# Kernel optimization log

Hardware: AMD Instinct MI355X
Metric: run time of the kernel (lower is better)

## Reference

```python
import jax, jax.numpy as jnp
import numpy as np

CK = 16          # ck_size
REP50 = 50       # extra_feature.repeat(1, 50)
BN_EPS = 1e-5
SLOPE = 0.01     # LeakyReLU default slope

def leaky(x):
    return jnp.where(x >= 0, x, SLOPE * x)

def bn(x):
    # BatchNorm1d(affine=False, track_running_stats=False): per-call batch stats
    m = jnp.mean(x, axis=0, keepdims=True)
    v = jnp.var(x, axis=0, keepdims=True)
    return (x - m) * jax.lax.rsqrt(v + BN_EPS)

def rev_within(x, lengths):
    # reverse each sequence within its valid length, keep padding in place
    B, T, _ = x.shape
    t = jnp.arange(T)[None, :]
    idx = jnp.where(t < lengths[:, None], lengths[:, None] - 1 - t, t)
    return jnp.take_along_axis(x, idx[:, :, None], axis=1)

def lstm(x, lengths, Wih, Whh, bih, bhh):
    # masked unidirectional LSTM; padded steps output zeros (pad_packed behavior)
    B, T, D = x.shape
    H = Whh.shape[1]
    xg = jnp.einsum('btd,gd->btg', x, Wih) + bih + bhh             # [B,T,4H]
    mask = (jnp.arange(T)[None, :] < lengths[:, None])[..., None]  # [B,T,1]
    def step(carry, inp):
        h, c = carry
        g, m = inp
        g = g + h @ Whh.T
        i, f, gg, o = jnp.split(g, 4, axis=-1)  # torch gate order i,f,g,o
        c_new = jax.nn.sigmoid(f) * c + jax.nn.sigmoid(i) * jnp.tanh(gg)
        h_new = jax.nn.sigmoid(o) * jnp.tanh(c_new)
        h = jnp.where(m, h_new, h)
        c = jnp.where(m, c_new, c)
        return (h, c), h_new * m
    init = (jnp.zeros((B, H), x.dtype), jnp.zeros((B, H), x.dtype))
    _, outs = jax.lax.scan(step, init, (xg.transpose(1, 0, 2), mask.transpose(1, 0, 2)))
    return outs.transpose(1, 0, 2)  # [B,T,H]

def att_var(inputs, lengths, s1_w, s1_b, s2_w):
    # NOTE: faithful to source softmax_by_length, which (due to the original
    # code) normalizes the *raw* masked logits linearly; exp() is discarded.
    B, T, D = inputs.shape
    utt = leaky(bn(inputs.reshape(-1, D) @ s1_w.T + s1_b))
    alpha = (utt @ s2_w.T).reshape(B, T)
    m = (jnp.arange(T)[None, :] < lengths[:, None]).astype(alpha.dtype)
    am = alpha * m
    alpha_ = am / (jnp.sum(am, axis=1, keepdims=True) + 1e-9)
    return jnp.einsum('bt,btd->bd', alpha_, inputs)

def item_att(x, y):
    # x: [D], y: [N, D] -> [N, 3D+1]
    xb = jnp.broadcast_to(x, y.shape)
    dist = jnp.linalg.norm(xb - y, axis=-1, keepdims=True)
    return jnp.concatenate([xb, y, dist, xb * y], axis=-1)


def setup_inputs() -> dict:
    key = jax.random.key(0)
    ks = jax.random.split(key, 30)
    D, T, B = 1024, 128, 256
    Ne, Nc, P = 64, 128, 50
    Hh = D // 2
    f32 = jnp.float32
    def rn(k, shape, s=0.05):
        return jax.random.normal(k, shape, f32) * s
    inp = {}
    inp['word_encode'] = jax.random.normal(ks[0], (B, T, D), f32)
    inp['pos_encode'] = jax.random.normal(ks[1], (Ne, Nc // CK, P), f32)
    inp['dis_encode'] = jax.random.normal(ks[2], (Ne, Nc, P), f32)
    sl = jax.random.randint(ks[3], (B,), T // 2, T + 1)
    inp['sen_lengths'] = sl.at[0].set(T)
    inp['label3'] = jax.random.randint(ks[4], (Ne, 3), -1, Nc)
    inp['emo_idx'] = jnp.arange(Ne)
    inp['cau_idx'] = jnp.arange(Ne, Ne + Nc)
    # BiLSTM params (torch layout: [4H, in])
    inp['Wih_f'] = rn(ks[5], (4 * Hh, D)); inp['Whh_f'] = rn(ks[6], (4 * Hh, Hh))
    inp['bih_f'] = rn(ks[7], (4 * Hh,));  inp['bhh_f'] = rn(ks[8], (4 * Hh,))
    inp['Wih_b'] = rn(ks[9], (4 * Hh, D)); inp['Whh_b'] = rn(ks[10], (4 * Hh, Hh))
    inp['bih_b'] = rn(ks[11], (4 * Hh,)); inp['bhh_b'] = rn(ks[12], (4 * Hh,))
    # attention / projection params
    inp['s1_w'] = rn(ks[13], (D, D)); inp['s1_b'] = rn(ks[14], (D,))
    inp['s2_w'] = rn(ks[15], (1, D))
    inp['W2_w'] = rn(ks[16], (D, 3 * D + 1 + P)); inp['W2_b'] = rn(ks[17], (D,))
    inp['Wo_w'] = rn(ks[18], (2, D)); inp['Wo_b'] = rn(ks[19], (2,))
    inp['W3_w'] = rn(ks[20], (D, 3 * D + 51 + P)); inp['W3_b'] = rn(ks[21], (D,))
    inp['cls_w'] = rn(ks[22], (2, D)); inp['cls_b'] = rn(ks[23], (2,))
    return inp


def reference(word_encode, pos_encode, dis_encode,
              Wih_f, Whh_f, bih_f, bhh_f, Wih_b, Whh_b, bih_b, bhh_b,
              s1_w, s1_b, s2_w, W2_w, W2_b, Wo_w, Wo_b, W3_w, W3_b, cls_w, cls_b,
              sen_lengths, label3, emo_idx, cau_idx):
    lengths = sen_lengths
    out_f = lstm(word_encode, lengths, Wih_f, Whh_f, bih_f, bhh_f)
    out_b = rev_within(lstm(rev_within(word_encode, lengths), lengths,
                            Wih_b, Whh_b, bih_b, bhh_b), lengths)
    Hseq = jnp.concatenate([out_f, out_b], axis=-1)          # [B,T,D]
    U = att_var(Hseq, lengths, s1_w, s1_b, s2_w)             # [B,D]
    text_emo = U[emo_idx]                                    # [Ne,D]
    text_cau = U[cau_idx]                                    # [Nc,D]
    Nc, D = text_cau.shape
    Ne = text_emo.shape[0]
    cau_chunks = text_cau.reshape(Nc // CK, CK, D)           # [Nck,CK,D]

    # ground-truth cause labels per emotion (label3 -> binary over cau utts)
    valid = (label3 >= 0)
    safe = jnp.where(valid, label3, 0)
    L = jnp.zeros((Ne, Nc), U.dtype).at[jnp.arange(Ne)[:, None], safe].max(valid.astype(U.dtype))

    def per_emo(emo, pos_j, dis_j):
        # phase-2: chunk-level attention + classification
        sc = jax.nn.softmax(jnp.einsum('d,ncd->nc', emo, cau_chunks), axis=1)
        chunkEmb = jnp.einsum('nc,ncd->nd', sc, cau_chunks)          # [Nck,D]
        delta = jnp.concatenate([item_att(emo, chunkEmb), pos_j], -1)
        hidden = leaky(bn(delta @ W2_w.T + W2_b))
        out2 = jax.nn.log_softmax(hidden @ Wo_w.T + Wo_b, axis=-1)   # [Nck,2]
        # phase-3: utterance-level with chunk prediction as extra feature
        extra = jnp.repeat(jnp.argmax(out2, axis=-1).astype(emo.dtype), CK)[:, None]
        delta_ = jnp.concatenate([item_att(emo, text_cau), dis_j,
                                  jnp.tile(extra, (1, REP50))], -1)
        h = leaky(bn(delta_ @ W3_w.T + W3_b))
        p = jax.nn.log_softmax(h @ cls_w.T + cls_b, axis=-1)         # [Nc,2]
        return out2, p

    phase2, p3 = jax.vmap(per_emo)(text_emo, pos_encode, dis_encode)
    return phase2, p3, L
```

## Files before the change

kernel.cpp:

```cpp
#include <hip/hip_runtime.h>
#include <math.h>

#define DD    1024
#define TT    128
#define BB    256
#define NE    64
#define NCC   128
#define PPP   50
#define NCK   8
#define HH    512
#define G4    2048
#define NROWS 32768
#define K3PAD 3200
#define CHUNK 8

#define F_HSEQ  0ull
#define F_XG    33554432ull
#define F_WIH   41943040ull
#define F_WHH   46137344ull
#define F_S1    48234496ull
#define F_W2    49283072ull
#define F_W3    52559872ull
#define F_BIASC 56885248ull
#define F_HST   56889344ull
#define F_CST   57413632ull
#define F_CS    57675776ull
#define F_CSQ   57676800ull
#define F_BNM   57677824ull
#define F_BNI   57678848ull
#define F_ALPHA 57679872ull
#define F_U     57712640ull
#define F_H2    57974784ull
#define F_BN2M  58499072ull
#define F_BN2I  58564608ull
#define F_EXTRA 58630144ull
#define F_BN3M  58631168ull
#define F_BN3I  58696704ull

#define F_D2    F_HSEQ
#define F_CHE   (F_HSEQ + 26214400ull)
#define F_D3    F_HSEQ
#define F_H3    F_XG

typedef short s8v __attribute__((ext_vector_type(8)));
typedef float f4v __attribute__((ext_vector_type(4)));

__device__ __forceinline__ float leakyf(float x) { return x >= 0.f ? x : 0.01f * x; }
__device__ __forceinline__ float sigmf(float x)  { return 1.f / (1.f + __expf(-x)); }
__device__ __forceinline__ float tanhfast(float x) {
  float e = __expf(2.f * x);
  return 1.f - 2.f / (e + 1.f);
}

__device__ __forceinline__ float blk_sum(float v, float* s4) {
  for (int o = 32; o > 0; o >>= 1) v += __shfl_down(v, o);
  __syncthreads();
  if ((threadIdx.x & 63) == 0) s4[threadIdx.x >> 6] = v;
  __syncthreads();
  return s4[0] + s4[1] + s4[2] + s4[3];
}

__device__ __forceinline__ void cvt2(float x0, float x1, unsigned& hi, unsigned& lo) {
  unsigned b0 = __float_as_uint(x0), b1 = __float_as_uint(x1);
  hi = (b0 >> 16) | (b1 & 0xffff0000u);
  float h0 = __uint_as_float(b0 & 0xffff0000u);
  float h1 = __uint_as_float(b1 & 0xffff0000u);
  unsigned l0 = __float_as_uint(x0 - h0);
  unsigned l1 = __float_as_uint(x1 - h1);
  lo = (l0 >> 16) | (l1 & 0xffff0000u);
}

__global__ __launch_bounds__(256) void k_cvt(const float* __restrict__ src,
                                             unsigned short* __restrict__ hi,
                                             unsigned short* __restrict__ lo,
                                             int Ks, int Kd) {
  int n = blockIdx.x;
  for (int k = threadIdx.x; k < Kd; k += 256) {
    float v = (k < Ks) ? src[(size_t)n * Ks + k] : 0.f;
    unsigned b = __float_as_uint(v);
    float h = __uint_as_float(b & 0xffff0000u);
    hi[(size_t)n * Kd + k] = (unsigned short)(b >> 16);
    lo[(size_t)n * Kd + k] = (unsigned short)(__float_as_uint(v - h) >> 16);
  }
}

__global__ __launch_bounds__(256) void k_biasc(const float* __restrict__ bf1, const float* __restrict__ bf2,
                                               const float* __restrict__ bb1, const float* __restrict__ bb2,
                                               float* __restrict__ out) {
  int i = blockIdx.x * 256 + threadIdx.x;
  if (i < G4) out[i] = bf1[i] + bf2[i];
  else        out[i] = bb1[i - G4] + bb2[i - G4];
}

template <int MODE>
__global__ __launch_bounds__(256, 2) void k_mf(
    const float* __restrict__ A,
    const unsigned short* __restrict__ Ahi, const unsigned short* __restrict__ Alo,
    const unsigned short* __restrict__ Bhi, const unsigned short* __restrict__ Blo,
    const float* __restrict__ bias, float* __restrict__ C, int M, int N, int K,
    const int* __restrict__ lens, int c,
    const float* __restrict__ bnm, const float* __restrict__ bni,
    const float* __restrict__ s2w, float* __restrict__ cs,
    float* __restrict__ csq, float* __restrict__ alpha) {
  __shared__ unsigned short Ah[128][40];
  __shared__ unsigned short Al[128][40];
  __shared__ unsigned short Bh[128][40];
  __shared__ unsigned short Bl[128][40];
  const int tid = threadIdx.x;
  const int m0 = blockIdx.x * 128;
  const int n0 = blockIdx.y * 128;
  const int dir = (MODE == 3) ? blockIdx.z : 0;

  const int sr = tid >> 1;
  const int sh = tid & 1;
  const float* arow = nullptr;
  const unsigned short* ahrow = nullptr;
  const unsigned short* alrow = nullptr;
  if (MODE == 3) {
    int tl = m0 >> 8;
    int b = (m0 & 255) + sr;
    int t = c * CHUNK + tl;
    int len = lens[b];
    int r = (dir == 0) ? t : ((t < len) ? (len - 1 - t) : t);
    arow = A + ((size_t)b * TT + r) * DD;
  } else if (MODE == 0) {
    arow = A + (size_t)(m0 + sr) * K;
  } else {
    ahrow = Ahi + (size_t)(m0 + sr) * K;
    alrow = Alo + (size_t)(m0 + sr) * K;
  }
  const unsigned short* bhrow = Bhi + ((size_t)dir * N + n0 + sr) * K;
  const unsigned short* blrow = Blo + ((size_t)dir * N + n0 + sr) * K;

  const int wave = tid >> 6, lane = tid & 63;
  const int wm = wave & 1, wn = wave >> 1;
  const int quad = lane >> 4, l15 = lane & 15;

  f4v acc[4][4];
#pragma unroll
  for (int i = 0; i < 4; ++i)
#pragma unroll
    for (int j = 0; j < 4; ++j) acc[i][j] = (f4v){0.f, 0.f, 0.f, 0.f};

#pragma unroll 1
  for (int k0 = 0; k0 < K; k0 += 32) {
    __syncthreads();
    if (MODE == 1 || MODE == 2) {
      const uint4* ph = (const uint4*)(ahrow + k0 + sh * 16);
      uint4* dh = (uint4*)&Ah[sr][sh * 16];
      dh[0] = ph[0]; dh[1] = ph[1];
      const uint4* pl = (const uint4*)(alrow + k0 + sh * 16);
      uint4* dl = (uint4*)&Al[sr][sh * 16];
      dl[0] = pl[0]; dl[1] = pl[1];
    } else {
      const float4* pa = (const float4*)(arow + k0 + sh * 16);
      float4 v0 = pa[0], v1 = pa[1], v2 = pa[2], v3 = pa[3];
      unsigned h[8], l[8];
      cvt2(v0.x, v0.y, h[0], l[0]); cvt2(v0.z, v0.w, h[1], l[1]);
      cvt2(v1.x, v1.y, h[2], l[2]); cvt2(v1.z, v1.w, h[3], l[3]);
      cvt2(v2.x, v2.y, h[4], l[4]); cvt2(v2.z, v2.w, h[5], l[5]);
      cvt2(v3.x, v3.y, h[6], l[6]); cvt2(v3.z, v3.w, h[7], l[7]);
      uint4* dh = (uint4*)&Ah[sr][sh * 16];
      dh[0] = make_uint4(h[0], h[1], h[2], h[3]);
      dh[1] = make_uint4(h[4], h[5], h[6], h[7]);
      uint4* dl = (uint4*)&Al[sr][sh * 16];
      dl[0] = make_uint4(l[0], l[1], l[2], l[3]);
      dl[1] = make_uint4(l[4], l[5], l[6], l[7]);
    }
    {
      const uint4* pbh = (const uint4*)(bhrow + k0 + sh * 16);
      uint4* dbh = (uint4*)&Bh[sr][sh * 16];
      dbh[0] = pbh[0]; dbh[1] = pbh[1];
      const uint4* pbl = (const uint4*)(blrow + k0 + sh * 16);
      uint4* dbl = (uint4*)&Bl[sr][sh * 16];
      dbl[0] = pbl[0]; dbl[1] = pbl[1];
    }
    __syncthreads();
    s8v ah[4], al[4], bh[4], bl[4];
#pragma unroll
    for (int mi = 0; mi < 4; ++mi) {
      ah[mi] = *(const s8v*)&Ah[wm * 64 + mi * 16 + l15][quad * 8];
      al[mi] = *(const s8v*)&Al[wm * 64 + mi * 16 + l15][quad * 8];
    }
#pragma unroll
    for (int ni = 0; ni < 4; ++ni) {
      bh[ni] = *(const s8v*)&Bh[wn * 64 + ni * 16 + l15][quad * 8];
      bl[ni] = *(const s8v*)&Bl[wn * 64 + ni * 16 + l15][quad * 8];
    }
#pragma unroll
    for (int mi = 0; mi < 4; ++mi)
#pragma unroll
      for (int ni = 0; ni < 4; ++ni) {
        acc[mi][ni] = __builtin_amdgcn_mfma_f32_16x16x32_bf16(ah[mi], bh[ni], acc[mi][ni], 0, 0, 0);
        acc[mi][ni] = __builtin_amdgcn_mfma_f32_16x16x32_bf16(al[mi], bh[ni], acc[mi][ni], 0, 0, 0);
        acc[mi][ni] = __builtin_amdgcn_mfma_f32_16x16x32_bf16(ah[mi], bl[ni], acc[mi][ni], 0, 0, 0);
      }
  }

  const int rb = wm * 64;
  if (MODE == 0 || MODE == 3) {
    float* Cb;
    const float* bp = bias;
    if (MODE == 3) {
      int tl = m0 >> 8;
      Cb = C + (((size_t)dir * CHUNK + tl) * 256 + (m0 & 255)) * (size_t)N;
      bp = bias + (size_t)dir * N;
    } else {
      Cb = C + (size_t)m0 * N;
    }
#pragma unroll
    for (int mi = 0; mi < 4; ++mi)
#pragma unroll
      for (int ni = 0; ni < 4; ++ni) {
        int col = n0 + wn * 64 + ni * 16 + l15;
        float bv = bp[col];
#pragma unroll
        for (int r = 0; r < 4; ++r) {
          int row = rb + mi * 16 + quad * 4 + r;
          Cb[(size_t)row * N + col] = acc[mi][ni][r] + bv;
        }
      }
  } else if (MODE == 1) {
#pragma unroll
    for (int ni = 0; ni < 4; ++ni) {
      int col = n0 + wn * 64 + ni * 16 + l15;
      float bv = bias[col];
      float s = 0.f, q = 0.f;
#pragma unroll
      for (int mi = 0; mi < 4; ++mi)
#pragma unroll
        for (int r = 0; r < 4; ++r) {
          float z = acc[mi][ni][r] + bv;
          s += z;
          q += z * z;
        }
      s += __shfl_xor(s, 16); s += __shfl_xor(s, 32);
      q += __shfl_xor(q, 16); q += __shfl_xor(q, 32);
      if (quad == 0) {
        atomicAdd(&cs[col], s);
        atomicAdd(&csq[col], q);
      }
    }
  } else {
#pragma unroll
    for (int mi = 0; mi < 4; ++mi) {
      float rv[4] = {0.f, 0.f, 0.f, 0.f};
#pragma unroll
      for (int ni = 0; ni < 4; ++ni) {
        int col = n0 + wn * 64 + ni * 16 + l15;
        float bv = bias[col], mc = bnm[col], ic = bni[col], wc = s2w[col];
#pragma unroll
        for (int r = 0; r < 4; ++r) {
          float z = acc[mi][ni][r] + bv;
          rv[r] += leakyf((z - mc) * ic) * wc;
        }
      }
#pragma unroll
      for (int r = 0; r < 4; ++r) {
        float v = rv[r];
        v += __shfl_xor(v, 1); v += __shfl_xor(v, 2);
        v += __shfl_xor(v, 4); v += __shfl_xor(v, 8);
        if (l15 == 0) atomicAdd(&alpha[m0 + rb + mi * 16 + quad * 4 + r], v);
      }
    }
  }
}

__global__ __launch_bounds__(256, 1) void k_step(
    const unsigned short* __restrict__ Bhi, const unsigned short* __restrict__ Blo,
    const float* __restrict__ XG, const int* __restrict__ lens,
    unsigned short* __restrict__ Hpk,
    float* __restrict__ Cst,
    unsigned short* __restrict__ Hhi, unsigned short* __restrict__ Hlo,
    int t) {
  __shared__ unsigned short Bsh[64 * 512];
  __shared__ unsigned short Bsl[64 * 512];
  const int tid = threadIdx.x;
  const int id = blockIdx.x;
  const int g = id & 7;
  const int b0 = (g >> 1) * 64;
  const int dir = g & 1;
  const int j0 = (id >> 3) * 16;
  const int tl = t & (CHUNK - 1);
  const int rpar = t & 1, wpar = (t + 1) & 1;

  const int wave = tid >> 6, lane = tid & 63;
  const int quad = lane >> 4, l15 = lane & 15;
  const int j = j0 + l15;
  const int amrow = b0 + wave * 16 + l15;

  const unsigned short* Ab = Hpk + (((size_t)rpar * 2 + dir) * BB + amrow) * 1024;
  uint4 ahv[16], alv[16];
#pragma unroll
  for (int ks = 0; ks < 16; ++ks) {
    const uint4* p = (const uint4*)Ab + (size_t)(ks * 4 + quad) * 2;
    ahv[ks] = p[0];
    alv[ks] = p[1];
  }

  int bv[4], lenv[4];
  float cstate[4], xgv[4][4];
  size_t sidx[4];
#pragma unroll
  for (int r = 0; r < 4; ++r) {
    bv[r] = b0 + wave * 16 + quad * 4 + r;
    lenv[r] = lens[bv[r]];
    sidx[r] = ((size_t)dir * BB + bv[r]) * HH + j;
    cstate[r] = Cst[sidx[r]];
    size_t xgb = (((size_t)dir * CHUNK + tl) * BB + bv[r]) * (size_t)G4 + j;
#pragma unroll
    for (int gg = 0; gg < 4; ++gg) xgv[r][gg] = XG[xgb + (size_t)gg * HH];
  }

#pragma unroll
  for (int ii = 0; ii < 16; ++ii) {
    int i = ii * 256 + tid;
    int row = i >> 6, s = i & 63;
    int sp = s ^ (row & 7);
    int grow = dir * G4 + (row >> 4) * HH + j0 + (row & 15);
    ((uint4*)Bsh)[row * 64 + sp] = ((const uint4*)(Bhi + (size_t)grow * HH))[s];
    ((uint4*)Bsl)[row * 64 + sp] = ((const uint4*)(Blo + (size_t)grow * HH))[s];
  }
  __syncthreads();

  f4v acc[4];
#pragma unroll
  for (int gg = 0; gg < 4; ++gg) acc[gg] = (f4v){0.f, 0.f, 0.f, 0.f};
#pragma unroll
  for (int ks = 0; ks < 16; ++ks) {
    s8v ah = *(s8v*)&ahv[ks];
    s8v al = *(s8v*)&alv[ks];
#pragma unroll
    for (int gg = 0; gg < 4; ++gg) {
      int row = gg * 16 + l15;
      int sp = (ks * 4 + quad) ^ (l15 & 7);
      s8v bh = *(const s8v*)(Bsh + row * 512 + sp * 8);
      s8v bl = *(const s8v*)(Bsl + row * 512 + sp * 8);
      acc[gg] = __builtin_amdgcn_mfma_f32_16x16x32_bf16(ah, bh, acc[gg], 0, 0, 0);
      acc[gg] = __builtin_amdgcn_mfma_f32_16x16x32_bf16(al, bh, acc[gg], 0, 0, 0);
      acc[gg] = __builtin_amdgcn_mfma_f32_16x16x32_bf16(ah, bl, acc[gg], 0, 0, 0);
    }
  }

  unsigned short* Wb = Hpk + (((size_t)wpar * 2 + dir) * BB) * 1024;
  const unsigned short* Rb = Hpk + (((size_t)rpar * 2 + dir) * BB) * 1024;
  const int oj = (j >> 3) * 16 + (j & 7);
#pragma unroll
  for (int r = 0; r < 4; ++r) {
    size_t wi = (size_t)bv[r] * 1024 + oj;
    if (t < lenv[r]) {
      float gi = acc[0][r] + xgv[r][0];
      float gf = acc[1][r] + xgv[r][1];
      float gg = acc[2][r] + xgv[r][2];
      float go = acc[3][r] + xgv[r][3];
      float cn = sigmf(gf) * cstate[r] + sigmf(gi) * tanhfast(gg);
      float hn = sigmf(go) * tanhfast(cn);
      Cst[sidx[r]] = cn;
      unsigned hb = __float_as_uint(hn);
      unsigned short h16 = (unsigned short)(hb >> 16);
      unsigned short l16 =
          (unsigned short)(__float_as_uint(hn - __uint_as_float(hb & 0xffff0000u)) >> 16);
      Wb[wi] = h16;
      Wb[wi + 8] = l16;
      int ro = dir ? (lenv[r] - 1 - t) : t;
      size_t hidx = ((size_t)bv[r] * TT + ro) * DD + (size_t)dir * HH + j;
      Hhi[hidx] = h16;
      Hlo[hidx] = l16;
    } else {
      Wb[wi] = Rb[wi];
      Wb[wi + 8] = Rb[wi + 8];
      size_t hidx = ((size_t)bv[r] * TT + t) * DD + (size_t)dir * HH + j;
      Hhi[hidx] = 0;
      Hlo[hidx] = 0;
    }
  }
}

__global__ __launch_bounds__(256) void k_bnfinal(const float* __restrict__ cs, const float* __restrict__ csq,
                                                 float* __restrict__ bnm, float* __restrict__ bni, float invN) {
  int i = blockIdx.x * 256 + threadIdx.x;
  if (i < DD) {
    float m = cs[i] * invN;
    float v = csq[i] * invN - m * m;
    bnm[i] = m;
    bni[i] = rsqrtf(v + 1e-5f);
  }
}

__global__ __launch_bounds__(128) void k_asum(float* __restrict__ alpha, const int* __restrict__ lens) {
  int b = blockIdx.x;
  int t = threadIdx.x;
  int len = lens[b];
  float v = (t < len) ? alpha[b * TT + t] : 0.f;
  float s = v;
  for (int o = 32; o > 0; o >>= 1) s += __shfl_down(s, o);
  __shared__ float sw[2];
  if ((t & 63) == 0) sw[t >> 6] = s;
  __syncthreads();
  float S = sw[0] + sw[1] + 1e-9f;
  alpha[b * TT + t] = v / S;
}

__global__ __launch_bounds__(256) void k_U(const unsigned short* __restrict__ Hhi,
                                           const unsigned short* __restrict__ Hlo,
                                           const float* __restrict__ alpha,
                                           float* __restrict__ U) {
  int b = blockIdx.x;
  int tid = threadIdx.x;
  __shared__ float al[TT];
  if (tid < TT) al[tid] = alpha[b * TT + tid];
  __syncthreads();
  float4 s = make_float4(0.f, 0.f, 0.f, 0.f);
  size_t base = (size_t)b * TT * DD + tid * 4;
#pragma unroll 4
  for (int t = 0; t < TT; ++t) {
    float a = al[t];
    ushort4 hv = *(const ushort4*)(Hhi + base + (size_t)t * DD);
    ushort4 lv = *(const ushort4*)(Hlo + base + (size_t)t * DD);
    s.x += a * (__uint_as_float((unsigned)hv.x << 16) + __uint_as_float((unsigned)lv.x << 16));
    s.y += a * (__uint_as_float((unsigned)hv.y << 16) + __uint_as_float((unsigned)lv.y << 16));
    s.z += a * (__uint_as_float((unsigned)hv.z << 16) + __uint_as_float((unsigned)lv.z << 16));
    s.w += a * (__uint_as_float((unsigned)hv.w << 16) + __uint_as_float((unsigned)lv.w << 16));
  }
  *(float4*)(U + (size_t)b * DD + tid * 4) = s;
}

__global__ __launch_bounds__(256) void k_p2a(const float* __restrict__ U,
                                             const int* __restrict__ emoI,
                                             const int* __restrict__ cauI,
                                             float* __restrict__ chunkEmb) {
  int e = blockIdx.x;
  int tid = threadIdx.x;
  __shared__ float emoS[DD];
  __shared__ float sc[NCK][16];
  const float* Ue = U + (size_t)emoI[e] * DD;
  for (int i = tid; i < DD; i += 256) emoS[i] = Ue[i];
  __syncthreads();
  int w = tid >> 6, lane = tid & 63;
  for (int p = w; p < 128; p += 4) {
    const float* y = U + (size_t)cauI[p] * DD;
    float s = 0;
    for (int d = lane; d < DD; d += 64) s += emoS[d] * y[d];
    for (int o = 32; o > 0; o >>= 1) s += __shfl_down(s, o);
    if (lane == 0) sc[p >> 4][p & 15] = s;
  }
  __syncthreads();
  if (tid < NCK) {
    float mx = -1e30f;
    for (int c = 0; c < 16; ++c) mx = fmaxf(mx, sc[tid][c]);
    float sum = 0;
    for (int c = 0; c < 16; ++c) {
      float ev = __expf(sc[tid][c] - mx);
      sc[tid][c] = ev;
      sum += ev;
    }
    float inv = 1.f / sum;
    for (int c = 0; c < 16; ++c) sc[tid][c] *= inv;
  }
  __syncthreads();
  int d = tid * 4;
  for (int nn = 0; nn < NCK; ++nn) {
    float4 s = make_float4(0.f, 0.f, 0.f, 0.f);
    for (int c = 0; c < 16; ++c) {
      float wc = sc[nn][c];
      float4 y = *(const float4*)(U + (size_t)cauI[nn * 16 + c] * DD + d);
      s.x += wc * y.x; s.y += wc * y.y; s.z += wc * y.z; s.w += wc * y.w;
    }
    *(float4*)(chunkEmb + ((size_t)e * NCK + nn) * DD + d) = s;
  }
}

__global__ __launch_bounds__(256) void k_delta2(const float* __restrict__ U,
                                                const int* __restrict__ emoI,
                                                const float* __restrict__ chunkEmb,
                                                const float* __restrict__ pos,
                                                float* __restrict__ delta2) {
  int e = blockIdx.x >> 3, nn = blockIdx.x & 7;
  int tid = threadIdx.x;
  const float* emo = U + (size_t)emoI[e] * DD;
  const float* y = chunkEmb + ((size_t)e * NCK + nn) * DD;
  __shared__ float s4[4];
  float ds = 0;
  for (int d = tid; d < DD; d += 256) {
    float df = emo[d] - y[d];
    ds += df * df;
  }
  float dist = sqrtf(blk_sum(ds, s4));
  float* out = delta2 + ((size_t)e * NCK + nn) * K3PAD;
  for (int c = tid; c < K3PAD; c += 256) {
    float v;
    if (c < 1024) v = emo[c];
    else if (c < 2048) v = y[c - 1024];
    else if (c == 2048) v = dist;
    else if (c < 3073) { int d = c - 2049; v = emo[d] * y[d]; }
    else if (c < 3123) v = pos[((size_t)e * NCK + nn) * PPP + (c - 3073)];
    else v = 0.f;
    out[c] = v;
  }
}

__global__ __launch_bounds__(256) void k_bnstats(const float* __restrict__ X,
                                                 float* __restrict__ bm, float* __restrict__ bi, int R) {
  int gid = blockIdx.x * 256 + threadIdx.x;
  int e = gid >> 10, col = gid & 1023;
  const float* p = X + (size_t)e * R * DD + col;
  float s = 0, s2 = 0;
  for (int r = 0; r < R; ++r) {
    float v = p[(size_t)r * DD];
    s += v;
    s2 += v * v;
  }
  float m = s / R;
  float var = s2 / R - m * m;
  bm[gid] = m;
  bi[gid] = rsqrtf(var + 1e-5f);
}

__global__ __launch_bounds__(256) void k_out2(const float* __restrict__ h2,
                                              const float* __restrict__ bm, const float* __restrict__ bi,
                                              const float* __restrict__ Wo, const float* __restrict__ Wob,
                                              float* __restrict__ out, float* __restrict__ extraf) {
  int e = blockIdx.x >> 3, nn = blockIdx.x & 7;
  int tid = threadIdx.x;
  const float* row = h2 + ((size_t)e * NCK + nn) * DD;
  float l0 = 0, l1 = 0;
  for (int col = tid; col < DD; col += 256) {
    float h = leakyf((row[col] - bm[e * DD + col]) * bi[e * DD + col]);
    l0 += h * Wo[col];
    l1 += h * Wo[DD + col];
  }
  __shared__ float s4[4];
  l0 = blk_sum(l0, s4);
  l1 = blk_sum(l1, s4);
  if (tid == 0) {
    l0 += Wob[0];
    l1 += Wob[1];
    float mx = fmaxf(l0, l1);
    float lse = mx + logf(__expf(l0 - mx) + __expf(l1 - mx));
    out[((size_t)e * NCK + nn) * 2 + 0] = l0 - lse;
    out[((size_t)e * NCK + nn) * 2 + 1] = l1 - lse;
    extraf[e * NCK + nn] = (l1 > l0) ? 1.f : 0.f;
  }
}

__global__ __launch_bounds__(256) void k_delta3(const float* __restrict__ U,
                                                const int* __restrict__ emoI,
                                                const int* __restrict__ cauI,
                                                const float* __restrict__ dis,
                                                const float* __restrict__ extraf,
                                                float* __restrict__ delta3) {
  int e = blockIdx.x >> 7, c = blockIdx.x & 127;
  int tid = threadIdx.x;
  const float* emo = U + (size_t)emoI[e] * DD;
  const float* y = U + (size_t)cauI[c] * DD;
  __shared__ float s4[4];
  float ds = 0;
  for (int d = tid; d < DD; d += 256) {
    float df = emo[d] - y[d];
    ds += df * df;
  }
  float dist = sqrtf(blk_sum(ds, s4));
  float ex = extraf[e * NCK + (c >> 4)];
  float* out = delta3 + ((size_t)e * NCC + c) * K3PAD;
  for (int col = tid; col < K3PAD; col += 256) {
    float v;
    if (col < 1024) v = emo[col];
    else if (col < 2048) v = y[col - 1024];
    else if (col == 2048) v = dist;
    else if (col < 3073) { int d = col - 2049; v = emo[d] * y[d]; }
    else if (col < 3123) v = dis[((size_t)e * NCC + c) * PPP + (col - 3073)];
    else if (col < 3173) v = ex;
    else v = 0.f;
    out[col] = v;
  }
}

__global__ __launch_bounds__(256) void k_p3(const float* __restrict__ h3,
                                            const float* __restrict__ bm, const float* __restrict__ bi,
                                            const float* __restrict__ cw, const float* __restrict__ cb,
                                            float* __restrict__ out) {
  int e = blockIdx.x >> 7, c = blockIdx.x & 127;
  int tid = threadIdx.x;
  const float* row = h3 + ((size_t)e * NCC + c) * DD;
  float l0 = 0, l1 = 0;
  for (int col = tid; col < DD; col += 256) {
    float h = leakyf((row[col] - bm[e * DD + col]) * bi[e * DD + col]);
    l0 += h * cw[col];
    l1 += h * cw[DD + col];
  }
  __shared__ float s4[4];
  l0 = blk_sum(l0, s4);
  l1 = blk_sum(l1, s4);
  if (tid == 0) {
    l0 += cb[0];
    l1 += cb[1];
    float mx = fmaxf(l0, l1);
    float lse = mx + logf(__expf(l0 - mx) + __expf(l1 - mx));
    out[((size_t)e * NCC + c) * 2 + 0] = l0 - lse;
    out[((size_t)e * NCC + c) * 2 + 1] = l1 - lse;
  }
}

__global__ __launch_bounds__(256) void k_L(const int* __restrict__ lab, float* __restrict__ out) {
  int i = blockIdx.x * 256 + threadIdx.x;
  int e = i >> 7, c = i & 127;
  int a = lab[e * 3 + 0], b = lab[e * 3 + 1], d = lab[e * 3 + 2];
  out[i] = (a == c || b == c || d == c) ? 1.f : 0.f;
}

extern "C" void kernel_launch(void* const* d_in, const int* in_sizes, int n_in,
                              void* d_out, int out_size, void* d_ws, size_t ws_size,
                              hipStream_t stream) {
  (void)in_sizes; (void)n_in; (void)out_size; (void)ws_size;
  const float* X     = (const float*)d_in[0];
  const float* pos   = (const float*)d_in[1];
  const float* dis   = (const float*)d_in[2];
  const int*   lens  = (const int*)d_in[3];
  const int*   lab3  = (const int*)d_in[4];
  const int*   emoI  = (const int*)d_in[5];
  const int*   cauI  = (const int*)d_in[6];
  const float* Wih_f = (const float*)d_in[7];
  const float* Whh_f = (const float*)d_in[8];
  const float* bih_f = (const float*)d_in[9];
  const float* bhh_f = (const float*)d_in[10];
  const float* Wih_b = (const float*)d_in[11];
  const float* Whh_b = (const float*)d_in[12];
  const float* bih_b = (const float*)d_in[13];
  const float* bhh_b = (const float*)d_in[14];
  const float* s1w   = (const float*)d_in[15];
  const float* s1b   = (const float*)d_in[16];
  const float* s2w   = (const float*)d_in[17];
  const float* W2w   = (const float*)d_in[18];
  const float* W2b   = (const float*)d_in[19];
  const float* Wow   = (const float*)d_in[20];
  const float* Wob   = (const float*)d_in[21];
  const float* W3w   = (const float*)d_in[22];
  const float* W3b   = (const float*)d_in[23];
  const float* clsw  = (const float*)d_in[24];
  const float* clsb  = (const float*)d_in[25];
  float* ws = (float*)d_ws;
  float* out = (float*)d_out;

  unsigned short* Hhi = (unsigned short*)(ws + F_HSEQ);
  unsigned short* Hlo = Hhi + (size_t)NROWS * DD;
  unsigned short* WIHhi = (unsigned short*)(ws + F_WIH);
  unsigned short* WIHlo = WIHhi + (size_t)2 * 2048 * 1024;
  unsigned short* WHHhi = (unsigned short*)(ws + F_WHH);
  unsigned short* WHHlo = WHHhi + (size_t)2 * 2048 * 512;
  unsigned short* S1hi  = (unsigned short*)(ws + F_S1);
  unsigned short* S1lo  = S1hi + (size_t)1024 * 1024;
  unsigned short* W2hi  = (unsigned short*)(ws + F_W2);
  unsigned short* W2lo  = W2hi + (size_t)1024 * K3PAD;
  unsigned short* W3hi  = (unsigned short*)(ws + F_W3);
  unsigned short* W3lo  = W3hi + (size_t)1024 * K3PAD;
  unsigned short* Hpk   = (unsigned short*)(ws + F_HST);

  hipMemsetAsync(ws + F_HST, 0, (size_t)(524288 + 262144) * sizeof(float), stream);
  hipMemsetAsync(ws + F_CS, 0, (size_t)2048 * sizeof(float), stream);
  hipMemsetAsync(ws + F_ALPHA, 0, (size_t)32768 * sizeof(float), stream);

  k_cvt<<<2048, 256, 0, stream>>>(Wih_f, WIHhi, WIHlo, 1024, 1024);
  k_cvt<<<2048, 256, 0, stream>>>(Wih_b, WIHhi + (size_t)2048 * 1024, WIHlo + (size_t)2048 * 1024, 1024, 1024);
  k_cvt<<<2048, 256, 0, stream>>>(Whh_f, WHHhi, WHHlo, 512, 512);
  k_cvt<<<2048, 256, 0, stream>>>(Whh_b, WHHhi + (size_t)2048 * 512, WHHlo + (size_t)2048 * 512, 512, 512);
  k_cvt<<<1024, 256, 0, stream>>>(s1w, S1hi, S1lo, 1024, 1024);
  k_cvt<<<1024, 256, 0, stream>>>(W2w, W2hi, W2lo, 3123, K3PAD);
  k_cvt<<<1024, 256, 0, stream>>>(W3w, W3hi, W3lo, 3173, K3PAD);
  k_biasc<<<16, 256, 0, stream>>>(bih_f, bhh_f, bih_b, bhh_b, ws + F_BIASC);

  for (int c = 0; c < TT / CHUNK; ++c) {
    k_mf<3><<<dim3(16, 16, 2), 256, 0, stream>>>(X, nullptr, nullptr, WIHhi, WIHlo,
                                                 ws + F_BIASC, ws + F_XG,
                                                 2048, 2048, 1024, lens, c,
                                                 nullptr, nullptr, nullptr, nullptr, nullptr, nullptr);
    for (int tt = 0; tt < CHUNK; ++tt) {
      int t = c * CHUNK + tt;
      k_step<<<dim3(256), 256, 0, stream>>>(WHHhi, WHHlo, ws + F_XG, lens,
                                            Hpk, ws + F_CST, Hhi, Hlo, t);
    }
  }

  k_mf<1><<<dim3(256, 8), 256, 0, stream>>>(nullptr, Hhi, Hlo, S1hi, S1lo, s1b, nullptr,
                                            NROWS, 1024, 1024, nullptr, 0,
                                            nullptr, nullptr, nullptr,
                                            ws + F_CS, ws + F_CSQ, nullptr);
  k_bnfinal<<<4, 256, 0, stream>>>(ws + F_CS, ws + F_CSQ, ws + F_BNM, ws + F_BNI, 1.f / NROWS);
  k_mf<2><<<dim3(256, 8), 256, 0, stream>>>(nullptr, Hhi, Hlo, S1hi, S1lo, s1b, nullptr,
                                            NROWS, 1024, 1024, nullptr, 0,
                                            ws + F_BNM, ws + F_BNI, s2w,
                                            nullptr, nullptr, ws + F_ALPHA);
  k_asum<<<BB, TT, 0, stream>>>(ws + F_ALPHA, lens);
  k_U<<<BB, 256, 0, stream>>>(Hhi, Hlo, ws + F_ALPHA, ws + F_U);

  k_p2a<<<NE, 256, 0, stream>>>(ws + F_U, emoI, cauI, ws + F_CHE);
  k_delta2<<<NE * NCK, 256, 0, stream>>>(ws + F_U, emoI, ws + F_CHE, pos, ws + F_D2);
  k_mf<0><<<dim3(4, 8), 256, 0, stream>>>(ws + F_D2, nullptr, nullptr, W2hi, W2lo, W2b, ws + F_H2,
                                          512, 1024, K3PAD, nullptr, 0,
                                          nullptr, nullptr, nullptr, nullptr, nullptr, nullptr);
  k_bnstats<<<256, 256, 0, stream>>>(ws + F_H2, ws + F_BN2M, ws + F_BN2I, NCK);
  k_out2<<<NE * NCK, 256, 0, stream>>>(ws + F_H2, ws + F_BN2M, ws + F_BN2I, Wow, Wob,
                                       out, ws + F_EXTRA);

  k_delta3<<<NE * NCC, 256, 0, stream>>>(ws + F_U, emoI, cauI, dis, ws + F_EXTRA, ws + F_D3);
  k_mf<0><<<dim3(64, 8), 256, 0, stream>>>(ws + F_D3, nullptr, nullptr, W3hi, W3lo, W3b, ws + F_H3,
                                           8192, 1024, K3PAD, nullptr, 0,
                                           nullptr, nullptr, nullptr, nullptr, nullptr, nullptr);
  k_bnstats<<<256, 256, 0, stream>>>(ws + F_H3, ws + F_BN3M, ws + F_BN3I, NCC);
  k_p3<<<NE * NCC, 256, 0, stream>>>(ws + F_H3, ws + F_BN3M, ws + F_BN3I, clsw, clsb, out + 1024);
  k_L<<<32, 256, 0, stream>>>(lab3, out + 17408);
}
```

Measured before the change: 4.028 ms.

## Factor W3 GEMM into shared emo/cau projections and restructure LSTM step kernel

The phase-3 GEMM over the materialised delta3 (K=3200) is split into two parts. The emo and cau projections are computed once per unique row (256 rows). A reduced K=1088 GEMM then builds the product, dis, dist and summed-extra columns on the fly and adds the precomputed projections in its epilogue. This removes writing and reading the large delta3 buffer and cuts redundant FLOPs. Separately, the LSTM step kernel now keeps Whh fragments in registers with a K-split across waves and an LDS reduction, instead of staging Whh through shared memory.

```diff
diff --git a/kernel.cpp b/kernel.cpp
--- a/kernel.cpp
+++ b/kernel.cpp
@@ -12,6 +12,7 @@
 #define G4    2048
 #define NROWS 32768
 #define K3PAD 3200
+#define KP3   1088
 #define CHUNK 8
 
 #define F_HSEQ  0ull
@@ -36,10 +37,10 @@
 #define F_EXTRA 58630144ull
 #define F_BN3M  58631168ull
 #define F_BN3I  58696704ull
+#define F_GIDX  58762240ull
 
 #define F_D2    F_HSEQ
 #define F_CHE   (F_HSEQ + 26214400ull)
-#define F_D3    F_HSEQ
 #define F_H3    F_XG
 
 typedef short s8v __attribute__((ext_vector_type(8)));
@@ -73,14 +74,33 @@
 __global__ __launch_bounds__(256) void k_cvt(const float* __restrict__ src,
                                              unsigned short* __restrict__ hi,
                                              unsigned short* __restrict__ lo,
-                                             int Ks, int Kd) {
+                                             int Ks, int Kd, int Sstride, int off) {
   int n = blockIdx.x;
   for (int k = threadIdx.x; k < Kd; k += 256) {
-    float v = (k < Ks) ? src[(size_t)n * Ks + k] : 0.f;
+    float v = (k < Ks) ? src[(size_t)n * Sstride + off + k] : 0.f;
     unsigned b = __float_as_uint(v);
     float h = __uint_as_float(b & 0xffff0000u);
     hi[(size_t)n * Kd + k] = (unsigned short)(b >> 16);
     lo[(size_t)n * Kd + k] = (unsigned short)(__float_as_uint(v - h) >> 16);
+  }
+}
+
+__global__ __launch_bounds__(256) void k_cvtp(const float* __restrict__ src,
+                                              unsigned short* __restrict__ hi,
+                                              unsigned short* __restrict__ lo) {
+  int o = blockIdx.x;
+  const float* s = src + (size_t)o * 3173;
+  for (int k = threadIdx.x; k < KP3; k += 256) {
+    float v;
+    if (k < 1024) v = s[2049 + k];
+    else if (k < 1074) v = s[3073 + (k - 1024)];
+    else if (k == 1074) v = s[2048];
+    else if (k == 1075) { float a = 0.f; for (int p = 0; p < 50; ++p) a += s[3123 + p]; v = a; }
+    else v = 0.f;
+    unsigned b = __float_as_uint(v);
+    float h = __uint_as_float(b & 0xffff0000u);
+    hi[(size_t)o * KP3 + k] = (unsigned short)(b >> 16);
+    lo[(size_t)o * KP3 + k] = (unsigned short)(__float_as_uint(v - h) >> 16);
   }
 }
 
@@ -90,6 +110,29 @@
   int i = blockIdx.x * 256 + threadIdx.x;
   if (i < G4) out[i] = bf1[i] + bf2[i];
   else        out[i] = bb1[i - G4] + bb2[i - G4];
+}
+
+__global__ __launch_bounds__(256) void k_gidx(const int* __restrict__ emoI, const int* __restrict__ cauI,
+                                              int* __restrict__ g) {
+  int i = threadIdx.x;
+  g[i] = (i < 64) ? emoI[i] : (i < 192 ? cauI[i - 64] : 0);
+}
+
+__global__ __launch_bounds__(256) void k_dist(const float* __restrict__ U,
+                                              const int* __restrict__ emoI, const int* __restrict__ cauI,
+                                              float* __restrict__ dist) {
+  int e = blockIdx.x >> 7, c = blockIdx.x & 127;
+  int tid = threadIdx.x;
+  const float* emo = U + (size_t)emoI[e] * DD;
+  const float* y = U + (size_t)cauI[c] * DD;
+  __shared__ float s4[4];
+  float ds = 0;
+  for (int d = tid; d < DD; d += 256) {
+    float df = emo[d] - y[d];
+    ds += df * df;
+  }
+  float dd = blk_sum(ds, s4);
+  if (tid == 0) dist[blockIdx.x] = sqrtf(dd);
 }
 
 template <int MODE>
@@ -101,7 +144,9 @@
     const int* __restrict__ lens, int c,
     const float* __restrict__ bnm, const float* __restrict__ bni,
     const float* __restrict__ s2w, float* __restrict__ cs,
-    float* __restrict__ csq, float* __restrict__ alpha) {
+    float* __restrict__ csq, float* __restrict__ alpha,
+    const int* __restrict__ gi1, const int* __restrict__ gi2,
+    const float* __restrict__ aux1, const float* __restrict__ aux2) {
   __shared__ unsigned short Ah[128][40];
   __shared__ unsigned short Al[128][40];
   __shared__ unsigned short Bh[128][40];
@@ -116,6 +161,8 @@
   const float* arow = nullptr;
   const unsigned short* ahrow = nullptr;
   const unsigned short* alrow = nullptr;
+  const float* emo5 = nullptr;
+  const float* y5 = nullptr;
   if (MODE == 3) {
     int tl = m0 >> 8;
     int b = (m0 & 255) + sr;
@@ -125,6 +172,11 @@
     arow = A + ((size_t)b * TT + r) * DD;
   } else if (MODE == 0) {
     arow = A + (size_t)(m0 + sr) * K;
+  } else if (MODE == 6) {
+    arow = A + (size_t)gi1[m0 + sr] * K;
+  } else if (MODE == 5) {
+    emo5 = A + (size_t)gi1[blockIdx.x] * DD;
+    y5   = A + (size_t)gi2[sr] * DD;
   } else {
     ahrow = Ahi + (size_t)(m0 + sr) * K;
     alrow = Alo + (size_t)(m0 + sr) * K;
@@ -152,6 +204,38 @@
       const uint4* pl = (const uint4*)(alrow + k0 + sh * 16);
       uint4* dl = (uint4*)&Al[sr][sh * 16];
       dl[0] = pl[0]; dl[1] = pl[1];
+    } else if (MODE == 5) {
+      unsigned h[8], l[8];
+      if (k0 < 1024) {
+        const float4* pe = (const float4*)(emo5 + k0 + sh * 16);
+        const float4* py = (const float4*)(y5 + k0 + sh * 16);
+        float4 a0 = pe[0], a1 = pe[1], a2 = pe[2], a3 = pe[3];
+        float4 b0 = py[0], b1 = py[1], b2 = py[2], b3 = py[3];
+        cvt2(a0.x * b0.x, a0.y * b0.y, h[0], l[0]); cvt2(a0.z * b0.z, a0.w * b0.w, h[1], l[1]);
+        cvt2(a1.x * b1.x, a1.y * b1.y, h[2], l[2]); cvt2(a1.z * b1.z, a1.w * b1.w, h[3], l[3]);
+        cvt2(a2.x * b2.x, a2.y * b2.y, h[4], l[4]); cvt2(a2.z * b2.z, a2.w * b2.w, h[5], l[5]);
+        cvt2(a3.x * b3.x, a3.y * b3.y, h[6], l[6]); cvt2(a3.z * b3.z, a3.w * b3.w, h[7], l[7]);
+      } else {
+        float v[16];
+#pragma unroll
+        for (int i = 0; i < 16; ++i) {
+          int k = k0 + sh * 16 + i;
+          float val;
+          if (k < 1074)      val = s2w[((size_t)blockIdx.x * NCC + sr) * PPP + (k - 1024)];
+          else if (k == 1074) val = aux1[blockIdx.x * NCC + sr];
+          else if (k == 1075) val = aux2[blockIdx.x * NCK + (sr >> 4)];
+          else               val = 0.f;
+          v[i] = val;
+        }
+#pragma unroll
+        for (int i = 0; i < 8; ++i) cvt2(v[2 * i], v[2 * i + 1], h[i], l[i]);
+      }
+      uint4* dh = (uint4*)&Ah[sr][sh * 16];
+      dh[0] = make_uint4(h[0], h[1], h[2], h[3]);
+      dh[1] = make_uint4(h[4], h[5], h[6], h[7]);
+      uint4* dl = (uint4*)&Al[sr][sh * 16];
+      dl[0] = make_uint4(l[0], l[1], l[2], l[3]);
+      dl[1] = make_uint4(l[4], l[5], l[6], l[7]);
     } else {
       const float4* pa = (const float4*)(arow + k0 + sh * 16);
       float4 v0 = pa[0], v1 = pa[1], v2 = pa[2], v3 = pa[3];
@@ -198,7 +282,7 @@
   }
 
   const int rb = wm * 64;
-  if (MODE == 0 || MODE == 3) {
+  if (MODE == 0 || MODE == 3 || MODE == 6) {
     float* Cb;
     const float* bp = bias;
     if (MODE == 3) {
@@ -213,11 +297,26 @@
 #pragma unroll
       for (int ni = 0; ni < 4; ++ni) {
         int col = n0 + wn * 64 + ni * 16 + l15;
-        float bv = bp[col];
+        float bv = (MODE == 6) ? 0.f : bp[col];
 #pragma unroll
         for (int r = 0; r < 4; ++r) {
           int row = rb + mi * 16 + quad * 4 + r;
           Cb[(size_t)row * N + col] = acc[mi][ni][r] + bv;
+        }
+      }
+  } else if (MODE == 5) {
+    float* Cb = C + (size_t)m0 * N;
+    int e5 = blockIdx.x;
+#pragma unroll
+    for (int mi = 0; mi < 4; ++mi)
+#pragma unroll
+      for (int ni = 0; ni < 4; ++ni) {
+        int col = n0 + wn * 64 + ni * 16 + l15;
+        float ev = bias[(size_t)e5 * 2048 + col] + bni[col];
+#pragma unroll
+        for (int r = 0; r < 4; ++r) {
+          int row = rb + mi * 16 + quad * 4 + r;
+          Cb[(size_t)row * N + col] = acc[mi][ni][r] + ev + bnm[(size_t)row * 2048 + col];
         }
       }
   } else if (MODE == 1) {
@@ -273,13 +372,12 @@
     float* __restrict__ Cst,
     unsigned short* __restrict__ Hhi, unsigned short* __restrict__ Hlo,
     int t) {
-  __shared__ unsigned short Bsh[64 * 512];
-  __shared__ unsigned short Bsl[64 * 512];
+  __shared__ f4v Red[4][4][4][64];
   const int tid = threadIdx.x;
   const int id = blockIdx.x;
-  const int g = id & 7;
-  const int b0 = (g >> 1) * 64;
-  const int dir = g & 1;
+  const int g7 = id & 7;
+  const int b0 = (g7 >> 1) * 64;
+  const int dir = g7 & 1;
   const int j0 = (id >> 3) * 16;
   const int tl = t & (CHUNK - 1);
   const int rpar = t & 1, wpar = (t + 1) & 1;
@@ -287,15 +385,30 @@
   const int wave = tid >> 6, lane = tid & 63;
   const int quad = lane >> 4, l15 = lane & 15;
   const int j = j0 + l15;
-  const int amrow = b0 + wave * 16 + l15;
-
-  const unsigned short* Ab = Hpk + (((size_t)rpar * 2 + dir) * BB + amrow) * 1024;
-  uint4 ahv[16], alv[16];
-#pragma unroll
-  for (int ks = 0; ks < 16; ++ks) {
-    const uint4* p = (const uint4*)Ab + (size_t)(ks * 4 + quad) * 2;
-    ahv[ks] = p[0];
-    alv[ks] = p[1];
+  const int kb = wave * 128;
+
+  uint4 bhv[4][4], blv[4][4];
+#pragma unroll
+  for (int g = 0; g < 4; ++g) {
+    size_t base = ((size_t)(dir * G4 + g * HH + j)) * HH + kb + quad * 8;
+#pragma unroll
+    for (int ks = 0; ks < 4; ++ks) {
+      bhv[g][ks] = *(const uint4*)(Bhi + base + ks * 32);
+      blv[g][ks] = *(const uint4*)(Blo + base + ks * 32);
+    }
+  }
+
+  const unsigned short* Ab = Hpk + (((size_t)rpar * 2 + dir) * BB) * 1024;
+  uint4 ahv[4][4], alv[4][4];
+#pragma unroll
+  for (int mi = 0; mi < 4; ++mi) {
+    const uint4* arow = (const uint4*)(Ab + (size_t)(b0 + mi * 16 + l15) * 1024)
+                        + (size_t)(wave * 16 + quad) * 2;
+#pragma unroll
+    for (int ks = 0; ks < 4; ++ks) {
+      ahv[mi][ks] = arow[ks * 8];
+      alv[mi][ks] = arow[ks * 8 + 1];
+    }
   }
 
   int bv[4], lenv[4];
@@ -312,35 +425,37 @@
     for (int gg = 0; gg < 4; ++gg) xgv[r][gg] = XG[xgb + (size_t)gg * HH];
   }
 
-#pragma unroll
-  for (int ii = 0; ii < 16; ++ii) {
-    int i = ii * 256 + tid;
-    int row = i >> 6, s = i & 63;
-    int sp = s ^ (row & 7);
-    int grow = dir * G4 + (row >> 4) * HH + j0 + (row & 15);
-    ((uint4*)Bsh)[row * 64 + sp] = ((const uint4*)(Bhi + (size_t)grow * HH))[s];
-    ((uint4*)Bsl)[row * 64 + sp] = ((const uint4*)(Blo + (size_t)grow * HH))[s];
-  }
+  f4v acc[4][4];
+#pragma unroll
+  for (int mi = 0; mi < 4; ++mi)
+#pragma unroll
+    for (int gg = 0; gg < 4; ++gg) acc[mi][gg] = (f4v){0.f, 0.f, 0.f, 0.f};
+#pragma unroll
+  for (int ks = 0; ks < 4; ++ks)
+#pragma unroll
+    for (int mi = 0; mi < 4; ++mi) {
+      s8v ah = *(s8v*)&ahv[mi][ks];
+      s8v al = *(s8v*)&alv[mi][ks];
+#pragma unroll
+      for (int gg = 0; gg < 4; ++gg) {
+        s8v bh = *(s8v*)&bhv[gg][ks];
+        s8v bl = *(s8v*)&blv[gg][ks];
+        acc[mi][gg] = __builtin_amdgcn_mfma_f32_16x16x32_bf16(ah, bh, acc[mi][gg], 0, 0, 0);
+        acc[mi][gg] = __builtin_amdgcn_mfma_f32_16x16x32_bf16(al, bh, acc[mi][gg], 0, 0, 0);
+        acc[mi][gg] = __builtin_amdgcn_mfma_f32_16x16x32_bf16(ah, bl, acc[mi][gg], 0, 0, 0);
+      }
+    }
+
+#pragma unroll
+  for (int mi = 0; mi < 4; ++mi)
+#pragma unroll
+    for (int gg = 0; gg < 4; ++gg) Red[wave][mi][gg][lane] = acc[mi][gg];
   __syncthreads();
-
-  f4v acc[4];
-#pragma unroll
-  for (int gg = 0; gg < 4; ++gg) acc[gg] = (f4v){0.f, 0.f, 0.f, 0.f};
-#pragma unroll
-  for (int ks = 0; ks < 16; ++ks) {
-    s8v ah = *(s8v*)&ahv[ks];
-    s8v al = *(s8v*)&alv[ks];
-#pragma unroll
-    for (int gg = 0; gg < 4; ++gg) {
-      int row = gg * 16 + l15;
-      int sp = (ks * 4 + quad) ^ (l15 & 7);
-      s8v bh = *(const s8v*)(Bsh + row * 512 + sp * 8);
-      s8v bl = *(const s8v*)(Bsl + row * 512 + sp * 8);
-      acc[gg] = __builtin_amdgcn_mfma_f32_16x16x32_bf16(ah, bh, acc[gg], 0, 0, 0);
-      acc[gg] = __builtin_amdgcn_mfma_f32_16x16x32_bf16(al, bh, acc[gg], 0, 0, 0);
-      acc[gg] = __builtin_amdgcn_mfma_f32_16x16x32_bf16(ah, bl, acc[gg], 0, 0, 0);
-    }
-  }
+  f4v fac[4];
+#pragma unroll
+  for (int gg = 0; gg < 4; ++gg)
+    fac[gg] = Red[0][wave][gg][lane] + Red[1][wave][gg][lane] +
+              Red[2][wave][gg][lane] + Red[3][wave][gg][lane];
 
   unsigned short* Wb = Hpk + (((size_t)wpar * 2 + dir) * BB) * 1024;
   const unsigned short* Rb = Hpk + (((size_t)rpar * 2 + dir) * BB) * 1024;
@@ -349,10 +464,10 @@
   for (int r = 0; r < 4; ++r) {
     size_t wi = (size_t)bv[r] * 1024 + oj;
     if (t < lenv[r]) {
-      float gi = acc[0][r] + xgv[r][0];
-      float gf = acc[1][r] + xgv[r][1];
-      float gg = acc[2][r] + xgv[r][2];
-      float go = acc[3][r] + xgv[r][3];
+      float gi = fac[0][r] + xgv[r][0];
+      float gf = fac[1][r] + xgv[r][1];
+      float gg = fac[2][r] + xgv[r][2];
+      float go = fac[3][r] + xgv[r][3];
       float cn = sigmf(gf) * cstate[r] + sigmf(gi) * tanhfast(gg);
       float hn = sigmf(go) * tanhfast(cn);
       Cst[sidx[r]] = cn;
@@ -540,38 +655,6 @@
     out[((size_t)e * NCK + nn) * 2 + 0] = l0 - lse;
     out[((size_t)e * NCK + nn) * 2 + 1] = l1 - lse;
     extraf[e * NCK + nn] = (l1 > l0) ? 1.f : 0.f;
-  }
-}
-
-__global__ __launch_bounds__(256) void k_delta3(const float* __restrict__ U,
-                                                const int* __restrict__ emoI,
-                                                const int* __restrict__ cauI,
-                                                const float* __restrict__ dis,
-                                                const float* __restrict__ extraf,
-                                                float* __restrict__ delta3) {
-  int e = blockIdx.x >> 7, c = blockIdx.x & 127;
-  int tid = threadIdx.x;
-  const float* emo = U + (size_t)emoI[e] * DD;
-  const float* y = U + (size_t)cauI[c] * DD;
-  __shared__ float s4[4];
-  float ds = 0;
-  for (int d = tid; d < DD; d += 256) {
-    float df = emo[d] - y[d];
-    ds += df * df;
-  }
-  float dist = sqrtf(blk_sum(ds, s4));
-  float ex = extraf[e * NCK + (c >> 4)];
-  float* out = delta3 + ((size_t)e * NCC + c) * K3PAD;
-  for (int col = tid; col < K3PAD; col += 256) {
-    float v;
-    if (col < 1024) v = emo[col];
-    else if (col < 2048) v = y[col - 1024];
-    else if (col == 2048) v = dist;
-    else if (col < 3073) { int d = col - 2049; v = emo[d] * y[d]; }
-    else if (col < 3123) v = dis[((size_t)e * NCC + c) * PPP + (col - 3073)];
-    else if (col < 3173) v = ex;
-    else v = 0.f;
-    out[col] = v;
   }
 }
 
@@ -651,28 +734,37 @@
   unsigned short* S1lo  = S1hi + (size_t)1024 * 1024;
   unsigned short* W2hi  = (unsigned short*)(ws + F_W2);
   unsigned short* W2lo  = W2hi + (size_t)1024 * K3PAD;
-  unsigned short* W3hi  = (unsigned short*)(ws + F_W3);
-  unsigned short* W3lo  = W3hi + (size_t)1024 * K3PAD;
+  unsigned short* W3ABhi = (unsigned short*)(ws + F_W3);
+  unsigned short* W3ABlo = W3ABhi + (size_t)2048 * 1024;
+  unsigned short* W3Phi  = (unsigned short*)(ws + F_W3 + 2097152ull);
+  unsigned short* W3Plo  = W3Phi + (size_t)1024 * KP3;
   unsigned short* Hpk   = (unsigned short*)(ws + F_HST);
+  float* E3Y3 = ws + F_H2;
+  float* distb = ws + F_ALPHA;
+  int* gidx = (int*)(ws + F_GIDX);
 
   hipMemsetAsync(ws + F_HST, 0, (size_t)(524288 + 262144) * sizeof(float), stream);
   hipMemsetAsync(ws + F_CS, 0, (size_t)2048 * sizeof(float), stream);
   hipMemsetAsync(ws + F_ALPHA, 0, (size_t)32768 * sizeof(float), stream);
 
-  k_cvt<<<2048, 256, 0, stream>>>(Wih_f, WIHhi, WIHlo, 1024, 1024);
-  k_cvt<<<2048, 256, 0, stream>>>(Wih_b, WIHhi + (size_t)2048 * 1024, WIHlo + (size_t)2048 * 1024, 1024, 1024);
-  k_cvt<<<2048, 256, 0, stream>>>(Whh_f, WHHhi, WHHlo, 512, 512);
-  k_cvt<<<2048, 256, 0, stream>>>(Whh_b, WHHhi + (size_t)2048 * 512, WHHlo + (size_t)2048 * 512, 512, 512);
-  k_cvt<<<1024, 256, 0, stream>>>(s1w, S1hi, S1lo, 1024, 1024);
-  k_cvt<<<1024, 256, 0, stream>>>(W2w, W2hi, W2lo, 3123, K3PAD);
-  k_cvt<<<1024, 256, 0, stream>>>(W3w, W3hi, W3lo, 3173, K3PAD);
+  k_cvt<<<2048, 256, 0, stream>>>(Wih_f, WIHhi, WIHlo, 1024, 1024, 1024, 0);
+  k_cvt<<<2048, 256, 0, stream>>>(Wih_b, WIHhi + (size_t)2048 * 1024, WIHlo + (size_t)2048 * 1024, 1024, 1024, 1024, 0);
+  k_cvt<<<2048, 256, 0, stream>>>(Whh_f, WHHhi, WHHlo, 512, 512, 512, 0);
+  k_cvt<<<2048, 256, 0, stream>>>(Whh_b, WHHhi + (size_t)2048 * 512, WHHlo + (size_t)2048 * 512, 512, 512, 512, 0);
+  k_cvt<<<1024, 256, 0, stream>>>(s1w, S1hi, S1lo, 1024, 1024, 1024, 0);
+  k_cvt<<<1024, 256, 0, stream>>>(W2w, W2hi, W2lo, 3123, K3PAD, 3123, 0);
+  k_cvt<<<1024, 256, 0, stream>>>(W3w, W3ABhi, W3ABlo, 1024, 1024, 3173, 0);
+  k_cvt<<<1024, 256, 0, stream>>>(W3w, W3ABhi + (size_t)1024 * 1024, W3ABlo + (size_t)1024 * 1024, 1024, 1024, 3173, 1024);
+  k_cvtp<<<1024, 256, 0, stream>>>(W3w, W3Phi, W3Plo);
   k_biasc<<<16, 256, 0, stream>>>(bih_f, bhh_f, bih_b, bhh_b, ws + F_BIASC);
+  k_gidx<<<1, 256, 0, stream>>>(emoI, cauI, gidx);
 
   for (int c = 0; c < TT / CHUNK; ++c) {
     k_mf<3><<<dim3(16, 16, 2), 256, 0, stream>>>(X, nullptr, nullptr, WIHhi, WIHlo,
                                                  ws + F_BIASC, ws + F_XG,
                                                  2048, 2048, 1024, lens, c,
-                                                 nullptr, nullptr, nullptr, nullptr, nullptr, nullptr);
+                                                 nullptr, nullptr, nullptr, nullptr, nullptr, nullptr,
+                                                 nullptr, nullptr, nullptr, nullptr);
     for (int tt = 0; tt < CHUNK; ++tt) {
       int t = c * CHUNK + tt;
       k_step<<<dim3(256), 256, 0, stream>>>(WHHhi, WHHlo, ws + F_XG, lens,
@@ -683,12 +775,14 @@
   k_mf<1><<<dim3(256, 8), 256, 0, stream>>>(nullptr, Hhi, Hlo, S1hi, S1lo, s1b, nullptr,
                                             NROWS, 1024, 1024, nullptr, 0,
                                             nullptr, nullptr, nullptr,
-                                            ws + F_CS, ws + F_CSQ, nullptr);
+                                            ws + F_CS, ws + F_CSQ, nullptr,
+                                            nullptr, nullptr, nullptr, nullptr);
   k_bnfinal<<<4, 256, 0, stream>>>(ws + F_CS, ws + F_CSQ, ws + F_BNM, ws + F_BNI, 1.f / NROWS);
   k_mf<2><<<dim3(256, 8), 256, 0, stream>>>(nullptr, Hhi, Hlo, S1hi, S1lo, s1b, nullptr,
                                             NROWS, 1024, 1024, nullptr, 0,
                                             ws + F_BNM, ws + F_BNI, s2w,
-                                            nullptr, nullptr, ws + F_ALPHA);
+                                            nullptr, nullptr, ws + F_ALPHA,
+                                            nullptr, nullptr, nullptr, nullptr);
   k_asum<<<BB, TT, 0, stream>>>(ws + F_ALPHA, lens);
   k_U<<<BB, 256, 0, stream>>>(Hhi, Hlo, ws + F_ALPHA, ws + F_U);
 
@@ -696,15 +790,22 @@
   k_delta2<<<NE * NCK, 256, 0, stream>>>(ws + F_U, emoI, ws + F_CHE, pos, ws + F_D2);
   k_mf<0><<<dim3(4, 8), 256, 0, stream>>>(ws + F_D2, nullptr, nullptr, W2hi, W2lo, W2b, ws + F_H2,
                                           512, 1024, K3PAD, nullptr, 0,
-                                          nullptr, nullptr, nullptr, nullptr, nullptr, nullptr);
+                                          nullptr, nullptr, nullptr, nullptr, nullptr, nullptr,
+                                          nullptr, nullptr, nullptr, nullptr);
   k_bnstats<<<256, 256, 0, stream>>>(ws + F_H2, ws + F_BN2M, ws + F_BN2I, NCK);
   k_out2<<<NE * NCK, 256, 0, stream>>>(ws + F_H2, ws + F_BN2M, ws + F_BN2I, Wow, Wob,
                                        out, ws + F_EXTRA);
 
-  k_delta3<<<NE * NCC, 256, 0, stream>>>(ws + F_U, emoI, cauI, dis, ws + F_EXTRA, ws + F_D3);
-  k_mf<0><<<dim3(64, 8), 256, 0, stream>>>(ws + F_D3, nullptr, nullptr, W3hi, W3lo, W3b, ws + F_H3,
-                                           8192, 1024, K3PAD, nullptr, 0,
-                                           nullptr, nullptr, nullptr, nullptr, nullptr, nullptr);
+  k_dist<<<NE * NCC, 256, 0, stream>>>(ws + F_U, emoI, cauI, distb);
+  k_mf<6><<<dim3(2, 16), 256, 0, stream>>>(ws + F_U, nullptr, nullptr, W3ABhi, W3ABlo,
+                                           nullptr, E3Y3, 256, 2048, 1024, nullptr, 0,
+                                           nullptr, nullptr, nullptr, nullptr, nullptr, nullptr,
+                                           gidx, nullptr, nullptr, nullptr);
+  k_mf<5><<<dim3(64, 8), 256, 0, stream>>>(ws + F_U, nullptr, nullptr, W3Phi, W3Plo,
+                                           E3Y3, ws + F_H3, 8192, 1024, KP3, nullptr, 0,
+                                           E3Y3 + (size_t)64 * 2048 + 1024, W3b, dis,
+                                           nullptr, nullptr, nullptr,
+                                           emoI, cauI, distb, ws + F_EXTRA);
   k_bnstats<<<256, 256, 0, stream>>>(ws + F_H3, ws + F_BN3M, ws + F_BN3I, NCC);
   k_p3<<<NE * NCC, 256, 0, stream>>>(ws + F_H3, ws + F_BN3M, ws + F_BN3I, clsw, clsb, out + 1024);
   k_L<<<32, 256, 0, stream>>>(lab3, out + 17408);
```

Result: faster. 3.890 ms (-3.4%).
